# Optimization experiments

Measured on AMD Instinct MI355X. Metric: run time of the kernel, lower is better.

Reference implementation:

```python
import jax, jax.numpy as jnp
import numpy as np

D = 1024
EPS = 1e-5  # torch LayerNorm default


def setup_inputs() -> dict:
    key = jax.random.key(0)
    ks = jax.random.split(key, 10)
    B, S = 4, 2048
    s = 1.0 / np.sqrt(D)
    inp = {
        "x": jax.random.normal(ks[0], (B, S, D), dtype=jnp.float32),
        "gamma": jnp.ones((D,), jnp.float32),
        "beta": jnp.zeros((D,), jnp.float32),
        "Wq": jax.random.normal(ks[1], (D, D), jnp.float32) * s,
        "bq": jax.random.normal(ks[2], (D,), jnp.float32) * 0.01,
        "Wk": jax.random.normal(ks[3], (D, D), jnp.float32) * s,
        "bk": jax.random.normal(ks[4], (D,), jnp.float32) * 0.01,
        "Wv": jax.random.normal(ks[5], (D, D), jnp.float32) * s,
        "bv": jax.random.normal(ks[6], (D,), jnp.float32) * 0.01,
        "Wo": jax.random.normal(ks[7], (D, D), jnp.float32) * s,
        "bo": jax.random.normal(ks[8], (D,), jnp.float32) * 0.01,
    }
    return inp


def reference(x, gamma, beta, Wq, bq, Wk, bk, Wv, bv, Wo, bo):
    # Pre-LayerNorm
    mu = jnp.mean(x, axis=-1, keepdims=True)
    var = jnp.mean(jnp.square(x - mu), axis=-1, keepdims=True)
    xn = (x - mu) * jax.lax.rsqrt(var + EPS) * gamma + beta
    # QKV projections (torch Linear: y = x @ W.T + b)
    Q = jnp.einsum('bsd,ed->bse', xn, Wq) + bq
    K = jnp.einsum('bsd,ed->bse', xn, Wk) + bk
    V = jnp.einsum('bsd,ed->bse', xn, Wv) + bv
    # Single-head full attention, scaled by sqrt(D); dropout inactive (eval)
    scores = jnp.einsum('bqd,bkd->bqk', Q, K) / jnp.sqrt(jnp.float32(D))
    attn = jax.nn.softmax(scores, axis=-1)
    out = jnp.einsum('bqk,bkd->bqd', attn, V)
    return jnp.einsum('bsd,ed->bse', out, Wo) + bo
```

## Files before the change

### kernel.cpp

```cpp
#include <hip/hip_runtime.h>
#include <hip/hip_bf16.h>
#include <stdint.h>

typedef __attribute__((ext_vector_type(4))) float f32x4;
typedef __attribute__((ext_vector_type(8))) __bf16 bf16x8;
typedef __attribute__((ext_vector_type(8))) unsigned short ushort8;

#define DEV static __device__ __forceinline__

__device__ __align__(4096) unsigned char g_scratch[96600064];

DEV unsigned short f2bf(float f) {
  union { float f; uint32_t u; } x; x.f = f;
  uint32_t u = x.u;
  uint32_t r = (u + 0x7fffu + ((u >> 16) & 1u)) >> 16;
  return (unsigned short)r;
}
DEV float bf2f(unsigned short b) {
  union { uint32_t u; float f; } x; x.u = ((uint32_t)b) << 16;
  return x.f;
}

DEV void gload16(const void* g, void* l) {
  __builtin_amdgcn_global_load_lds((const __attribute__((address_space(1))) void*)g,
                                   (__attribute__((address_space(3))) void*)l,
                                   16, 0, 0);
}

DEV int swz(int b) { return b ^ (((b >> 7) & 7) << 4); }

DEV void gemm_core(const unsigned short* a_t, const unsigned short* b_t,
                   int ldA, int ldB, int K, unsigned short* lds, int tid,
                   const int* aOff, const int* bOff, f32x4 acc[4][4])
{
  for (int kt = 0; kt < K; kt += 64) {
#pragma unroll
    for (int i = 0; i < 4; ++i) {
      int o = i * 4096 + tid * 16;
      int p = swz(o);
      int row = p >> 7;
      int ce  = (p & 127) >> 1;
      gload16(a_t + (size_t)row * ldA + (kt + ce), (char*)lds + o);
      gload16(b_t + (size_t)row * ldB + (kt + ce), (char*)lds + 16384 + o);
    }
    __syncthreads();
#pragma unroll
    for (int h = 0; h < 2; ++h) {
      bf16x8 av[4], bv4[4];
#pragma unroll
      for (int m = 0; m < 4; ++m)
        av[m] = *(const bf16x8*)((const char*)lds + (aOff[m] ^ (h << 6)));
#pragma unroll
      for (int n = 0; n < 4; ++n)
        bv4[n] = *(const bf16x8*)((const char*)lds + (bOff[n] ^ (h << 6)));
#pragma unroll
      for (int m = 0; m < 4; ++m)
#pragma unroll
        for (int n = 0; n < 4; ++n)
          acc[m][n] = __builtin_amdgcn_mfma_f32_16x16x32_bf16(av[m], bv4[n], acc[m][n], 0, 0, 0);
    }
    __syncthreads();
  }
}

DEV void frag_offsets(int lane, int wm, int wn, int* aOff, int* bOff)
{
#pragma unroll
  for (int m = 0; m < 4; ++m) {
    int ar = wm + m * 16 + (lane & 15);
    aOff[m] = (ar * 128 + ((lane >> 4) * 16)) ^ ((ar & 7) << 4);
    int br = wn + m * 16 + (lane & 15);
    bOff[m] = ((br * 128 + ((lane >> 4) * 16)) ^ ((br & 7) << 4)) + 16384;
  }
}

__global__ __launch_bounds__(256, 4)
void g0(const unsigned short* __restrict__ wkT, const unsigned short* __restrict__ wqT,
        const unsigned short* __restrict__ woB, const unsigned short* __restrict__ wvT,
        unsigned short* __restrict__ mt, unsigned short* __restrict__ w4)
{
  __shared__ unsigned short lds[16384];
  const int tid = threadIdx.x, lane = tid & 63, wave = tid >> 6;
  const int z = blockIdx.z;
  const int m0 = blockIdx.x * 128, n0 = blockIdx.y * 128;
  const int wm = (wave >> 1) * 64, wn = (wave & 1) * 64;
  int aOff[4], bOff[4];
  frag_offsets(lane, wm, wn, aOff, bOff);
  f32x4 acc[4][4] = {};
  const unsigned short* a_t = (z == 0) ? (wkT + (size_t)m0 * 1024) : (woB + (size_t)m0 * 1024);
  const unsigned short* b_t = (z == 0) ? (wqT + (size_t)n0 * 1024) : (wvT + (size_t)n0 * 1024);
  gemm_core(a_t, b_t, 1024, 1024, 1024, lds, tid, aOff, bOff, acc);

  const int r0 = (lane >> 4) * 4, cL = lane & 15;
  const float scale = (z == 0) ? 0.03125f : 1.0f;
  unsigned short* Cp = (z == 0) ? mt : w4;
#pragma unroll
  for (int n = 0; n < 4; ++n) {
    int colg = n0 + wn + n * 16 + cL;
#pragma unroll
    for (int m = 0; m < 4; ++m) {
      int rowg = m0 + wm + m * 16 + r0;
#pragma unroll
      for (int i = 0; i < 4; ++i)
        Cp[(size_t)(rowg + i) * 1024 + colg] = f2bf(acc[m][n][i] * scale);
    }
  }
}

__global__ __launch_bounds__(256, 4)
void g1(const unsigned short* __restrict__ xn, const unsigned short* __restrict__ mt,
        const unsigned short* __restrict__ w4, unsigned short* __restrict__ Z,
        unsigned short* __restrict__ yt)
{
  __shared__ unsigned short lds[16384];
  const int tid = threadIdx.x, lane = tid & 63, wave = tid >> 6;
  const int z = blockIdx.z;
  const int m0 = blockIdx.x * 128, n0 = blockIdx.y * 128;
  const int wm = (wave >> 1) * 64, wn = (wave & 1) * 64;
  int aOff[4], bOff[4];
  frag_offsets(lane, wm, wn, aOff, bOff);
  f32x4 acc[4][4] = {};
  const unsigned short* b_t = ((z == 0) ? mt : w4) + (size_t)n0 * 1024;
  gemm_core(xn + (size_t)m0 * 1024, b_t, 1024, 1024, 1024, lds, tid, aOff, bOff, acc);

  const int r0 = (lane >> 4) * 4, cL = lane & 15;
  if (z == 0) {
#pragma unroll
    for (int n = 0; n < 4; ++n) {
      int colg = n0 + wn + n * 16 + cL;
#pragma unroll
      for (int m = 0; m < 4; ++m) {
        int rowg = m0 + wm + m * 16 + r0;
#pragma unroll
        for (int i = 0; i < 4; ++i)
          Z[(size_t)(rowg + i) * 1024 + colg] = f2bf(acc[m][n][i]);
      }
    }
  } else {
#pragma unroll
    for (int n = 0; n < 4; ++n) {
      int colg = n0 + wn + n * 16 + cL;
#pragma unroll
      for (int m = 0; m < 4; ++m) {
        int rowg = m0 + wm + m * 16 + r0;
        int bat = rowg >> 11, sdx = rowg & 2047;
        ushort4 pk;
        pk.x = f2bf(acc[m][n][0]);
        pk.y = f2bf(acc[m][n][1]);
        pk.z = f2bf(acc[m][n][2]);
        pk.w = f2bf(acc[m][n][3]);
        *(ushort4*)(yt + (size_t)bat * 2097152 + (size_t)colg * 2048 + sdx) = pk;
      }
    }
  }
}

__global__ __launch_bounds__(256, 4)
void g2(const unsigned short* __restrict__ Z, const unsigned short* __restrict__ xn,
        unsigned short* __restrict__ S, const float* __restrict__ w,
        float* __restrict__ rsum)
{
  __shared__ unsigned short lds[16384];
  const int tid = threadIdx.x, lane = tid & 63, wave = tid >> 6;
  const int z = blockIdx.z;
  const int m0 = blockIdx.x * 128, n0 = blockIdx.y * 128;
  const int wm = (wave >> 1) * 64, wn = (wave & 1) * 64;
  int aOff[4], bOff[4];
  frag_offsets(lane, wm, wn, aOff, bOff);
  f32x4 acc[4][4] = {};
  gemm_core(Z + (size_t)z * 2097152 + (size_t)m0 * 1024,
            xn + (size_t)z * 2097152 + (size_t)n0 * 1024,
            1024, 1024, 1024, lds, tid, aOff, bOff, acc);

  const int r0 = (lane >> 4) * 4, cL = lane & 15;
  unsigned short* Cp = S + (size_t)z * 4194304;
  float rs[4][4];
#pragma unroll
  for (int m = 0; m < 4; ++m)
#pragma unroll
    for (int i = 0; i < 4; ++i) rs[m][i] = 0.0f;
#pragma unroll
  for (int n = 0; n < 4; ++n) {
    int colg = n0 + wn + n * 16 + cL;
    float wv = w[(size_t)z * 2048 + colg];
#pragma unroll
    for (int m = 0; m < 4; ++m) {
      int rowg = m0 + wm + m * 16 + r0;
#pragma unroll
      for (int i = 0; i < 4; ++i) {
        float p = __expf(acc[m][n][i] + wv - 12.0f);
        rs[m][i] += p;
        Cp[(size_t)(rowg + i) * 2048 + colg] = f2bf(p);
      }
    }
  }
#pragma unroll
  for (int m = 0; m < 4; ++m)
#pragma unroll
    for (int i = 0; i < 4; ++i) {
      float v = rs[m][i];
      v += __shfl_xor(v, 1);
      v += __shfl_xor(v, 2);
      v += __shfl_xor(v, 4);
      v += __shfl_xor(v, 8);
      if (cL == 0)
        atomicAdd(&rsum[(size_t)z * 2048 + m0 + wm + m * 16 + r0 + i], v);
    }
}

__global__ __launch_bounds__(256, 4)
void g3(const unsigned short* __restrict__ S, const unsigned short* __restrict__ yt,
        float* __restrict__ out, const float* __restrict__ bb,
        const float* __restrict__ rsum)
{
  __shared__ unsigned short lds[16384];
  const int tid = threadIdx.x, lane = tid & 63, wave = tid >> 6;
  const int z = blockIdx.z;
  const int m0 = blockIdx.x * 128, n0 = blockIdx.y * 128;
  const int wm = (wave >> 1) * 64, wn = (wave & 1) * 64;
  int aOff[4], bOff[4];
  frag_offsets(lane, wm, wn, aOff, bOff);
  f32x4 acc[4][4] = {};
  gemm_core(S + (size_t)z * 4194304 + (size_t)m0 * 2048,
            yt + (size_t)z * 2097152 + (size_t)n0 * 2048,
            2048, 2048, 2048, lds, tid, aOff, bOff, acc);

  const int r0 = (lane >> 4) * 4, cL = lane & 15;
  float* Cp = out + (size_t)z * 2097152;
#pragma unroll
  for (int m = 0; m < 4; ++m) {
    int rowg = m0 + wm + m * 16 + r0;
#pragma unroll
    for (int i = 0; i < 4; ++i) {
      float inv = 1.0f / rsum[(size_t)z * 2048 + rowg + i];
#pragma unroll
      for (int n = 0; n < 4; ++n) {
        int colg = n0 + wn + n * 16 + cL;
        Cp[(size_t)(rowg + i) * 1024 + colg] = acc[m][n][i] * inv + bb[colg];
      }
    }
  }
}

__global__ __launch_bounds__(256)
void prep(const float* __restrict__ x, const float* __restrict__ gamma,
          const float* __restrict__ beta, unsigned short* __restrict__ xn,
          const float* __restrict__ Wq, const float* __restrict__ Wk,
          const float* __restrict__ Wv, const float* __restrict__ Wo,
          const float* __restrict__ bq, const float* __restrict__ bv,
          const float* __restrict__ bo,
          unsigned short* __restrict__ wqT, unsigned short* __restrict__ wkT,
          unsigned short* __restrict__ wvT, unsigned short* __restrict__ woB,
          float* __restrict__ cvec, float* __restrict__ bb,
          float* __restrict__ rsm)
{
  __shared__ float tlds[64][65];
  const int bid = blockIdx.x;
  const int tid = threadIdx.x;

  if (bid < 8192) {
    const int row = bid;
    const float4 xv = ((const float4*)(x + (size_t)row * 1024))[tid];
    float s = xv.x + xv.y + xv.z + xv.w;
#pragma unroll
    for (int d = 1; d < 64; d <<= 1) s += __shfl_xor(s, d);
    __shared__ float red1[4], red2[4];
    const int lane = tid & 63, wv_ = tid >> 6;
    if (lane == 0) red1[wv_] = s;
    __syncthreads();
    const float mu = (red1[0] + red1[1] + red1[2] + red1[3]) * (1.0f / 1024.0f);
    float4 dv;
    dv.x = xv.x - mu; dv.y = xv.y - mu; dv.z = xv.z - mu; dv.w = xv.w - mu;
    float vs = dv.x * dv.x + dv.y * dv.y + dv.z * dv.z + dv.w * dv.w;
#pragma unroll
    for (int d = 1; d < 64; d <<= 1) vs += __shfl_xor(vs, d);
    if (lane == 0) red2[wv_] = vs;
    __syncthreads();
    const float var = (red2[0] + red2[1] + red2[2] + red2[3]) * (1.0f / 1024.0f);
    const float rs = rsqrtf(var + 1e-5f);
    const float4 g = ((const float4*)gamma)[tid];
    const float4 b = ((const float4*)beta)[tid];
    ushort4 o;
    o.x = f2bf(dv.x * rs * g.x + b.x);
    o.y = f2bf(dv.y * rs * g.y + b.y);
    o.z = f2bf(dv.z * rs * g.z + b.z);
    o.w = f2bf(dv.w * rs * g.w + b.w);
    ((ushort4*)(xn + (size_t)row * 1024))[tid] = o;
    return;
  }
  if (bid < 8704) {
    const int xb = bid - 8192;
    const int idx = (xb * 256 + tid) * 8;
    const float4 a = *(const float4*)(Wo + idx);
    const float4 b = *(const float4*)(Wo + idx + 4);
    ushort4 r0, r1;
    r0.x = f2bf(a.x); r0.y = f2bf(a.y); r0.z = f2bf(a.z); r0.w = f2bf(a.w);
    r1.x = f2bf(b.x); r1.y = f2bf(b.y); r1.z = f2bf(b.z); r1.w = f2bf(b.w);
    *(ushort4*)(woB + idx) = r0;
    *(ushort4*)(woB + idx + 4) = r1;
    return;
  }
  if (bid < 9472) {
    const int t = bid - 8704;
    const int mat = t >> 8;
    const int tile = t & 255;
    const int R0 = (tile >> 4) * 64, C0 = (tile & 15) * 64;
    const float* src = (mat == 0) ? Wq : (mat == 1) ? Wk : Wv;
    unsigned short* dst = (mat == 0) ? wqT : (mat == 1) ? wkT : wvT;
#pragma unroll
    for (int p = 0; p < 4; ++p) {
      int r = p * 16 + (tid >> 4);
      int c = (tid & 15) * 4;
      float4 v = *(const float4*)(src + (size_t)(R0 + r) * 1024 + C0 + c);
      tlds[r][c + 0] = v.x; tlds[r][c + 1] = v.y;
      tlds[r][c + 2] = v.z; tlds[r][c + 3] = v.w;
    }
    __syncthreads();
    const int c = tid >> 2;
    const int chunk = tid & 3;
    ushort8 o0, o1;
#pragma unroll
    for (int k = 0; k < 8; ++k)  o0[k] = f2bf(tlds[chunk * 16 + k][c]);
#pragma unroll
    for (int k = 0; k < 8; ++k)  o1[k] = f2bf(tlds[chunk * 16 + 8 + k][c]);
    unsigned short* dp = dst + (size_t)(C0 + c) * 1024 + R0 + chunk * 16;
    *(ushort8*)(dp) = o0;
    *(ushort8*)(dp + 8) = o1;
    return;
  }
  if (bid < 9476) {
    const int cb = bid - 9472;
    const int i2 = (cb * 256 + tid) * 2;
    ((float4*)rsm)[i2] = make_float4(0.f, 0.f, 0.f, 0.f);
    ((float4*)rsm)[i2 + 1] = make_float4(0.f, 0.f, 0.f, 0.f);
    const int d = cb * 256 + tid;
    float acc = 0.f;
    for (int e = 0; e < 1024; ++e)
      acc += Wk[(size_t)e * 1024 + d] * bq[e];
    cvec[d] = acc * 0.03125f;
    return;
  }
  {
    const int vb = bid - 9476;
    const int wv_ = tid >> 6, lane = tid & 63;
#pragma unroll 1
    for (int pass = 0; pass < 16; ++pass) {
      const int e = vb * 64 + wv_ * 16 + pass;
      float s = 0.f;
#pragma unroll
      for (int q = 0; q < 4; ++q) {
        float4 a = *(const float4*)(Wo + (size_t)e * 1024 + lane * 16 + q * 4);
        float4 b = *(const float4*)(bv + lane * 16 + q * 4);
        s += a.x * b.x + a.y * b.y + a.z * b.z + a.w * b.w;
      }
#pragma unroll
      for (int d = 1; d < 64; d <<= 1) s += __shfl_xor(s, d);
      if (lane == 0) bb[e] = s + bo[e];
    }
  }
}

__global__ __launch_bounds__(256)
void wkern(const unsigned short* __restrict__ xn, const float* __restrict__ cvec,
           float* __restrict__ w)
{
  const int tid = threadIdx.x, lane = tid & 63, wv_ = tid >> 6;
  const int j = blockIdx.x * 4 + wv_;
  float s = 0.f;
#pragma unroll
  for (int q = 0; q < 2; ++q) {
    ushort8 v = *(const ushort8*)(xn + (size_t)j * 1024 + lane * 16 + q * 8);
#pragma unroll
    for (int k = 0; k < 8; ++k)
      s += bf2f(v[k]) * cvec[lane * 16 + q * 8 + k];
  }
#pragma unroll
  for (int d = 1; d < 64; d <<= 1) s += __shfl_xor(s, d);
  if (lane == 0) w[j] = s;
}

extern "C" void kernel_launch(void* const* d_in, const int* in_sizes, int n_in,
                              void* d_out, int out_size, void* d_ws, size_t ws_size,
                              hipStream_t stream) {
  const float* x     = (const float*)d_in[0];
  const float* gamma = (const float*)d_in[1];
  const float* beta  = (const float*)d_in[2];
  const float* Wq    = (const float*)d_in[3];
  const float* bq    = (const float*)d_in[4];
  const float* Wk    = (const float*)d_in[5];
  const float* Wv    = (const float*)d_in[7];
  const float* bv    = (const float*)d_in[8];
  const float* Wo    = (const float*)d_in[9];
  const float* bo    = (const float*)d_in[10];

  char* ws;
  if (ws_size >= (size_t)96542720) {
    ws = (char*)d_ws;
  } else {
    void* sp = nullptr;
    hipGetSymbolAddress(&sp, HIP_SYMBOL(g_scratch));
    ws = (char*)sp;
  }

  unsigned short* xn  = (unsigned short*)(ws);
  unsigned short* Z   = (unsigned short*)(ws + 16777216);
  unsigned short* yt  = (unsigned short*)(ws + 33554432);
  unsigned short* S   = (unsigned short*)(ws + 50331648);
  unsigned short* wqT = (unsigned short*)(ws + 83886080);
  unsigned short* wkT = (unsigned short*)(ws + 85983232);
  unsigned short* wvT = (unsigned short*)(ws + 88080384);
  unsigned short* woB = (unsigned short*)(ws + 90177536);
  unsigned short* mt  = (unsigned short*)(ws + 92274688);
  unsigned short* w4  = (unsigned short*)(ws + 94371840);
  float*          wv_ = (float*)(ws + 96468992);
  float*          rsm = (float*)(ws + 96501760);
  float*          bb  = (float*)(ws + 96534528);
  float*          cv  = (float*)(ws + 96538624);

  prep<<<9492, 256, 0, stream>>>(x, gamma, beta, xn, Wq, Wk, Wv, Wo,
                                 bq, bv, bo, wqT, wkT, wvT, woB, cv, bb, rsm);
  wkern<<<2048, 256, 0, stream>>>(xn, cv, wv_);
  g0<<<dim3(8, 8, 2), 256, 0, stream>>>(wkT, wqT, woB, wvT, mt, w4);
  g1<<<dim3(64, 8, 2), 256, 0, stream>>>(xn, mt, w4, Z, yt);
  g2<<<dim3(16, 16, 4), 256, 0, stream>>>(Z, xn, S, wv_, rsm);
  g3<<<dim3(16, 8, 4), 256, 0, stream>>>(S, yt, (float*)d_out, bb, rsm);
}
```

Measured before the change: 189.1 us.

## Parallelize bias-vector GEMVs into aux kernel and fold w computation into g1

The serial per-thread Wk^T·bq loop (four blocks, each thread striding 1024 rows) and the 16-pass Wo·bv loop in prep move into a new aux kernel. There each wave reduces one row, reading the bf16 transposed Wk with coalesced loads. The separate wkern launch is removed and its row dot-products become an extra z-slice of g1, which saves a launch and overlaps that work with the GEMM. The cost is a little bf16 precision in cvec, since it now reads wkT instead of fp32 Wk, plus one extra small launch.

```diff
diff --git a/kernel.cpp b/kernel.cpp
--- a/kernel.cpp
+++ b/kernel.cpp
@@ -110,11 +110,33 @@
 __global__ __launch_bounds__(256, 4)
 void g1(const unsigned short* __restrict__ xn, const unsigned short* __restrict__ mt,
         const unsigned short* __restrict__ w4, unsigned short* __restrict__ Z,
-        unsigned short* __restrict__ yt)
+        unsigned short* __restrict__ yt, const float* __restrict__ cvec,
+        float* __restrict__ w)
 {
   __shared__ unsigned short lds[16384];
   const int tid = threadIdx.x, lane = tid & 63, wave = tid >> 6;
   const int z = blockIdx.z;
+
+  if (z == 2) {
+    const int flat = blockIdx.y * 64 + blockIdx.x;
+#pragma unroll
+    for (int p = 0; p < 4; ++p) {
+      const int j = flat * 16 + wave * 4 + p;
+      float s = 0.f;
+#pragma unroll
+      for (int q = 0; q < 2; ++q) {
+        ushort8 v = *(const ushort8*)(xn + (size_t)j * 1024 + lane * 16 + q * 8);
+#pragma unroll
+        for (int k = 0; k < 8; ++k)
+          s += bf2f(v[k]) * cvec[lane * 16 + q * 8 + k];
+      }
+#pragma unroll
+      for (int d = 1; d < 64; d <<= 1) s += __shfl_xor(s, d);
+      if (lane == 0) w[j] = s;
+    }
+    return;
+  }
+
   const int m0 = blockIdx.x * 128, n0 = blockIdx.y * 128;
   const int wm = (wave >> 1) * 64, wn = (wave & 1) * 64;
   int aOff[4], bOff[4];
@@ -247,12 +269,8 @@
           const float* __restrict__ beta, unsigned short* __restrict__ xn,
           const float* __restrict__ Wq, const float* __restrict__ Wk,
           const float* __restrict__ Wv, const float* __restrict__ Wo,
-          const float* __restrict__ bq, const float* __restrict__ bv,
-          const float* __restrict__ bo,
           unsigned short* __restrict__ wqT, unsigned short* __restrict__ wkT,
-          unsigned short* __restrict__ wvT, unsigned short* __restrict__ woB,
-          float* __restrict__ cvec, float* __restrict__ bb,
-          float* __restrict__ rsm)
+          unsigned short* __restrict__ wvT, unsigned short* __restrict__ woB)
 {
   __shared__ float tlds[64][65];
   const int bid = blockIdx.x;
@@ -300,7 +318,7 @@
     *(ushort4*)(woB + idx + 4) = r1;
     return;
   }
-  if (bid < 9472) {
+  {
     const int t = bid - 8704;
     const int mat = t >> 8;
     const int tile = t & 255;
@@ -326,57 +344,48 @@
     unsigned short* dp = dst + (size_t)(C0 + c) * 1024 + R0 + chunk * 16;
     *(ushort8*)(dp) = o0;
     *(ushort8*)(dp + 8) = o1;
-    return;
-  }
-  if (bid < 9476) {
-    const int cb = bid - 9472;
-    const int i2 = (cb * 256 + tid) * 2;
+  }
+}
+
+__global__ __launch_bounds__(256)
+void aux(const unsigned short* __restrict__ wkT, const float* __restrict__ bq,
+         const float* __restrict__ Wo, const float* __restrict__ bv,
+         const float* __restrict__ bo, float* __restrict__ cvec,
+         float* __restrict__ bb, float* __restrict__ rsm)
+{
+  const int bid = blockIdx.x, tid = threadIdx.x;
+  const int lane = tid & 63, wv_ = tid >> 6;
+  if (bid < 4) {
+    const int i2 = (bid * 256 + tid) * 2;
     ((float4*)rsm)[i2] = make_float4(0.f, 0.f, 0.f, 0.f);
     ((float4*)rsm)[i2 + 1] = make_float4(0.f, 0.f, 0.f, 0.f);
-    const int d = cb * 256 + tid;
-    float acc = 0.f;
-    for (int e = 0; e < 1024; ++e)
-      acc += Wk[(size_t)e * 1024 + d] * bq[e];
-    cvec[d] = acc * 0.03125f;
-    return;
-  }
-  {
-    const int vb = bid - 9476;
-    const int wv_ = tid >> 6, lane = tid & 63;
-#pragma unroll 1
-    for (int pass = 0; pass < 16; ++pass) {
-      const int e = vb * 64 + wv_ * 16 + pass;
-      float s = 0.f;
-#pragma unroll
-      for (int q = 0; q < 4; ++q) {
-        float4 a = *(const float4*)(Wo + (size_t)e * 1024 + lane * 16 + q * 4);
-        float4 b = *(const float4*)(bv + lane * 16 + q * 4);
-        s += a.x * b.x + a.y * b.y + a.z * b.z + a.w * b.w;
-      }
-#pragma unroll
-      for (int d = 1; d < 64; d <<= 1) s += __shfl_xor(s, d);
-      if (lane == 0) bb[e] = s + bo[e];
-    }
-  }
-}
-
-__global__ __launch_bounds__(256)
-void wkern(const unsigned short* __restrict__ xn, const float* __restrict__ cvec,
-           float* __restrict__ w)
-{
-  const int tid = threadIdx.x, lane = tid & 63, wv_ = tid >> 6;
-  const int j = blockIdx.x * 4 + wv_;
-  float s = 0.f;
-#pragma unroll
-  for (int q = 0; q < 2; ++q) {
-    ushort8 v = *(const ushort8*)(xn + (size_t)j * 1024 + lane * 16 + q * 8);
-#pragma unroll
-    for (int k = 0; k < 8; ++k)
-      s += bf2f(v[k]) * cvec[lane * 16 + q * 8 + k];
-  }
-#pragma unroll
-  for (int d = 1; d < 64; d <<= 1) s += __shfl_xor(s, d);
-  if (lane == 0) w[j] = s;
+  }
+  if (bid < 256) {
+    const int d = bid * 4 + wv_;
+    float s = 0.f;
+#pragma unroll
+    for (int q = 0; q < 2; ++q) {
+      ushort8 v = *(const ushort8*)(wkT + (size_t)d * 1024 + lane * 16 + q * 8);
+#pragma unroll
+      for (int k = 0; k < 8; ++k)
+        s += bf2f(v[k]) * bq[lane * 16 + q * 8 + k];
+    }
+#pragma unroll
+    for (int dd = 1; dd < 64; dd <<= 1) s += __shfl_xor(s, dd);
+    if (lane == 0) cvec[d] = s * 0.03125f;
+  } else {
+    const int e = (bid - 256) * 4 + wv_;
+    float s = 0.f;
+#pragma unroll
+    for (int q = 0; q < 4; ++q) {
+      float4 a = *(const float4*)(Wo + (size_t)e * 1024 + lane * 16 + q * 4);
+      float4 b = *(const float4*)(bv + lane * 16 + q * 4);
+      s += a.x * b.x + a.y * b.y + a.z * b.z + a.w * b.w;
+    }
+#pragma unroll
+    for (int dd = 1; dd < 64; dd <<= 1) s += __shfl_xor(s, dd);
+    if (lane == 0) bb[e] = s + bo[e];
+  }
 }
 
 extern "C" void kernel_launch(void* const* d_in, const int* in_sizes, int n_in,
@@ -417,11 +426,11 @@
   float*          bb  = (float*)(ws + 96534528);
   float*          cv  = (float*)(ws + 96538624);
 
-  prep<<<9492, 256, 0, stream>>>(x, gamma, beta, xn, Wq, Wk, Wv, Wo,
-                                 bq, bv, bo, wqT, wkT, wvT, woB, cv, bb, rsm);
-  wkern<<<2048, 256, 0, stream>>>(xn, cv, wv_);
+  prep<<<9472, 256, 0, stream>>>(x, gamma, beta, xn, Wq, Wk, Wv, Wo,
+                                 wqT, wkT, wvT, woB);
+  aux<<<512, 256, 0, stream>>>(wkT, bq, Wo, bv, bo, cv, bb, rsm);
   g0<<<dim3(8, 8, 2), 256, 0, stream>>>(wkT, wqT, woB, wvT, mt, w4);
-  g1<<<dim3(64, 8, 2), 256, 0, stream>>>(xn, mt, w4, Z, yt);
+  g1<<<dim3(64, 8, 3), 256, 0, stream>>>(xn, mt, w4, Z, yt, cv, wv_);
   g2<<<dim3(16, 16, 4), 256, 0, stream>>>(Z, xn, S, wv_, rsm);
   g3<<<dim3(16, 8, 4), 256, 0, stream>>>(S, yt, (float*)d_out, bb, rsm);
 }
```

Result: faster. 162.3 us (-14.2%).
